# Kernel tuning notes

Hardware: AMD Instinct MI355X
Metric: run time of the kernel (lower is better)

Reference implementation:

```python
import jax, jax.numpy as jnp
import numpy as np

K = 20  # neighbors

def setup_inputs() -> dict:
    key = jax.random.key(0)
    k1, k2 = jax.random.split(key)
    B, C, N, O = 8, 64, 4096, 64
    x = jax.random.normal(k1, (B, C, N), dtype=jnp.float32)
    W = jax.random.normal(k2, (O, 2 * C), dtype=jnp.float32) * (1.0 / np.sqrt(2 * C))
    b = jnp.zeros((O,), dtype=jnp.float32)
    return {"x": x, "W": W, "b": b}

def _knn_idx(pts, k):
    # pts: [B, N, d]; returns [B, N, k] indices of k nearest neighbors (incl. self)
    sq = jnp.sum(pts * pts, axis=-1)                      # [B, N]
    inner = jnp.einsum('bnd,bmd->bnm', pts, pts)          # [B, N, N]
    neg_d2 = 2.0 * inner - sq[:, :, None] - sq[:, None, :]
    _, idx = jax.lax.top_k(neg_d2, k)                     # largest -dist = nearest
    return idx

def reference(x, W, b):
    # x: [B, C, N], W: [O, 2C], b: [O]
    pts = jnp.transpose(x, (0, 2, 1))                     # [B, N, C]
    idx = _knn_idx(jax.lax.stop_gradient(pts), K)         # [B, N, K]
    nbr = jax.vmap(lambda p, i: p[i])(pts, idx)           # [B, N, K, C]
    ctr = pts[:, :, None, :]                              # [B, N, 1, C]
    # local+global edge features: [diff, center] along channel dim -> [B, N, K, 2C]
    edge = jnp.concatenate([nbr - ctr, jnp.broadcast_to(ctr, nbr.shape)], axis=-1)
    # 1x1 conv == channel GEMM
    out = jnp.einsum('bnkc,oc->bonk', edge, W) + b[None, :, None, None]
    return jnp.max(out, axis=-1)                          # [B, O, N]
```

## Files before the change

### kernel.cpp

```cpp
#include <hip/hip_runtime.h>
#include <float.h>

typedef unsigned long long u64;
typedef unsigned int u32;
typedef unsigned short u16;

#define NPTS 4096
#define CDIM 64
#define BATCH 8
#define KSEL 20

#define F_XTL (BATCH * NPTS * 32)
#define F_CAND (2 * BATCH * NPTS * 32)
#define F_XTF (4 * BATCH * NPTS * 32)
#define F_SQ (6 * BATCH * NPTS * 32)
#define F_WT2 (F_SQ + BATCH * NPTS)
#define F_SQB (F_WT2 + 64 * 64)

typedef __attribute__((ext_vector_type(8))) short short8v;
typedef __attribute__((ext_vector_type(16))) float float16v;

#define MFMA32(a, b, c) __builtin_amdgcn_mfma_f32_32x32x16_bf16(a, b, c, 0, 0, 0)

__device__ __forceinline__ u32 ordf(float f) {
    u32 u = __float_as_uint(f);
    return (u >> 31) ? ~u : (u | 0x80000000u);
}
__device__ __forceinline__ u32 umaxu(u32 a, u32 b) { return a > b ? a : b; }
__device__ __forceinline__ u32 uminu(u32 a, u32 b) { return a < b ? a : b; }

__device__ __forceinline__ void load_lds_16(const void* g, void* l) {
    __builtin_amdgcn_global_load_lds(
        (const __attribute__((address_space(1))) unsigned int*)g,
        (__attribute__((address_space(3))) unsigned int*)l, 16, 0, 0);
}

#define CE(i, j) { u32 a_ = c[i], b_ = c[j]; c[i] = umaxu(a_, b_); c[j] = uminu(a_, b_); }

__device__ __forceinline__ void sort16_desc(u32 (&c)[16]) {
    CE(0,1) CE(2,3) CE(4,5) CE(6,7) CE(8,9) CE(10,11) CE(12,13) CE(14,15)
    CE(0,2) CE(1,3) CE(4,6) CE(5,7) CE(8,10) CE(9,11) CE(12,14) CE(13,15)
    CE(1,2) CE(5,6) CE(9,10) CE(13,14)
    CE(0,4) CE(1,5) CE(2,6) CE(3,7) CE(8,12) CE(9,13) CE(10,14) CE(11,15)
    CE(2,4) CE(3,5) CE(10,12) CE(11,13)
    CE(1,2) CE(3,4) CE(5,6) CE(9,10) CE(11,12) CE(13,14)
    CE(0,8) CE(1,9) CE(2,10) CE(3,11) CE(4,12) CE(5,13) CE(6,14) CE(7,15)
    CE(4,8) CE(5,9) CE(6,10) CE(7,11)
    CE(2,4) CE(3,5) CE(6,8) CE(7,9) CE(10,12) CE(11,13)
    CE(1,2) CE(3,4) CE(5,6) CE(7,8) CE(9,10) CE(11,12) CE(13,14)
}
#undef CE

__device__ __forceinline__ void merge_into16(u32 (&L)[16], const u32 (&c)[16]) {
#pragma unroll
    for (int i = 0; i < 16; i++) L[i] = umaxu(L[i], c[15 - i]);
#pragma unroll
    for (int j = 8; j >= 1; j >>= 1)
#pragma unroll
        for (int i = 0; i < 16; i++)
            if ((i & j) == 0) {
                int p = i | j;
                u32 a = L[i], b = L[p];
                L[i] = umaxu(a, b);
                L[p] = uminu(a, b);
            }
}

__global__ __launch_bounds__(256) void p1_prep(const float* __restrict__ x,
                                               const float* __restrict__ W,
                                               float* __restrict__ xtf,
                                               u16* __restrict__ xth,
                                               u16* __restrict__ xtl,
                                               float* __restrict__ sq,
                                               float* __restrict__ sqb,
                                               float* __restrict__ wt2g) {
    __shared__ float Xp[64][65];
    int tid = threadIdx.x;
    if (blockIdx.x >= 512) {
        int f = (blockIdx.x - 512) * 256 + tid;
        if (f < 64 * 64) {
            int c = f >> 6, o = f & 63;
            wt2g[f] = W[o * 128 + 64 + c] - W[o * 128 + c];
        }
        return;
    }
    int b = blockIdx.x >> 6;
    int n0 = (blockIdx.x & 63) * 64;
    const float* xb = x + (size_t)b * (CDIM * NPTS);
    int j = tid & 63, cq = tid >> 6;
#pragma unroll
    for (int i = 0; i < 16; i++) {
        int c = cq * 16 + i;
        Xp[c][j] = xb[(size_t)c * NPTS + n0 + j];
    }
    __syncthreads();
    if (tid < 64) {
        float s = 0.f;
        for (int c = 0; c < 64; c++) { float v = Xp[c][tid]; s = fmaf(v, v, s); }
        sq[(size_t)b * NPTS + n0 + tid] = s;
        sqb[(size_t)b * NPTS + n0 + tid] = 1024.f - s;
    }
    int n = tid >> 2, c0 = (tid & 3) * 16;
    float vv[16];
#pragma unroll
    for (int i = 0; i < 16; i++) vv[i] = Xp[c0 + i][n];
    size_t rowb = ((size_t)b * NPTS + n0 + n) * 64 + c0;
#pragma unroll
    for (int q = 0; q < 4; q++) {
        float4 f;
        f.x = vv[4 * q]; f.y = vv[4 * q + 1]; f.z = vv[4 * q + 2]; f.w = vv[4 * q + 3];
        *(float4*)(xtf + rowb + 4 * q) = f;
    }
    u16 hb[16], lb[16];
#pragma unroll
    for (int i = 0; i < 16; i++) {
        float v = vv[i] * 1.41421356237f;
        u32 bv = __float_as_uint(v);
        u32 h = (bv + 0x7FFFu + ((bv >> 16) & 1u)) >> 16;
        float hf = __uint_as_float(h << 16);
        float lf = v - hf;
        u32 bl = __float_as_uint(lf);
        u32 lo = (bl + 0x7FFFu + ((bl >> 16) & 1u)) >> 16;
        hb[i] = (u16)h; lb[i] = (u16)lo;
    }
    uint4 H0, H1, L0, L1;
    H0.x = hb[0] | ((u32)hb[1] << 16);  H0.y = hb[2] | ((u32)hb[3] << 16);
    H0.z = hb[4] | ((u32)hb[5] << 16);  H0.w = hb[6] | ((u32)hb[7] << 16);
    H1.x = hb[8] | ((u32)hb[9] << 16);  H1.y = hb[10] | ((u32)hb[11] << 16);
    H1.z = hb[12] | ((u32)hb[13] << 16); H1.w = hb[14] | ((u32)hb[15] << 16);
    L0.x = lb[0] | ((u32)lb[1] << 16);  L0.y = lb[2] | ((u32)lb[3] << 16);
    L0.z = lb[4] | ((u32)lb[5] << 16);  L0.w = lb[6] | ((u32)lb[7] << 16);
    L1.x = lb[8] | ((u32)lb[9] << 16);  L1.y = lb[10] | ((u32)lb[11] << 16);
    L1.z = lb[12] | ((u32)lb[13] << 16); L1.w = lb[14] | ((u32)lb[15] << 16);
    *(uint4*)(xth + rowb) = H0;
    *(uint4*)(xth + rowb + 8) = H1;
    *(uint4*)(xtl + rowb) = L0;
    *(uint4*)(xtl + rowb + 8) = L1;
}

__device__ __forceinline__ void stage_tile(const u16* __restrict__ srcb,
                                           char* lds, int w, int lane) {
#pragma unroll
    for (int i = 0; i < 2; i++) {
        int G = w * 128 + i * 64 + lane;
        int rr = G >> 3, gp = G & 7;
        const u16* src = srcb + rr * 64 + ((gp ^ (rr & 7)) << 3);
        char* dst = lds + (w * 128 + i * 64) * 16;
        load_lds_16(src, dst);
    }
}

__device__ __forceinline__ void sel_half(const float16v& A, int colbase2,
                                         u32 (&L)[16]) {
    u32 c[16];
#pragma unroll
    for (int q = 0; q < 4; q++) {
        u32 cg = (u32)(colbase2 + 8 * q);
        c[4 * q + 0] = (__float_as_uint(A[4 * q + 0]) & 0xFFFFF000u) | (cg + 0);
        c[4 * q + 1] = (__float_as_uint(A[4 * q + 1]) & 0xFFFFF000u) | (cg + 1);
        c[4 * q + 2] = (__float_as_uint(A[4 * q + 2]) & 0xFFFFF000u) | (cg + 2);
        c[4 * q + 3] = (__float_as_uint(A[4 * q + 3]) & 0xFFFFF000u) | (cg + 3);
    }
    sort16_desc(c);
    merge_into16(L, c);
}

__global__ __launch_bounds__(256, 4) void k2_gram(const u16* __restrict__ xth,
                                                  const u16* __restrict__ xtl,
                                                  const float* __restrict__ sqb,
                                                  u32* __restrict__ cand) {
    __shared__ char pool[8192];
    int tid = threadIdx.x;
    int lane = tid & 63, w = tid >> 6;
    int l31 = lane & 31, lh = lane >> 5;
    int b = blockIdx.x & 7;
    int rt = (blockIdx.x >> 3) & 31;
    int ch = blockIdx.x >> 8;
    int r0 = rt * 128;
    int cb = ch * 1024;
    size_t bbase = (size_t)b * NPTS;

    short8v Ah[4], Al[4];
    {
        const u16* pa = xth + (bbase + r0 + 32 * w + l31) * 64 + 8 * lh;
        const u16* pl = xtl + (bbase + r0 + 32 * w + l31) * 64 + 8 * lh;
#pragma unroll
        for (int s = 0; s < 4; s++) {
            Ah[s] = *(const short8v*)(pa + 16 * s);
            Al[s] = *(const short8v*)(pl + 16 * s);
        }
    }

    u32 L[16];
#pragma unroll
    for (int i = 0; i < 16; i++) L[i] = 0u;

    stage_tile(xth + (bbase + cb) * 64, pool, w, lane);
    __syncthreads();

    for (int t = 0; t < 16; t++) {
        int n1 = cb + t * 64;
        const float* sqbp = sqb + bbase + n1 + 4 * lh;

        float16v a0, a1;
#pragma unroll
        for (int q = 0; q < 4; q++) {
            ((float4*)&a0)[q] = *(const float4*)(sqbp + 8 * q);
            ((float4*)&a1)[q] = *(const float4*)(sqbp + 32 + 8 * q);
        }

#pragma unroll
        for (int s = 0; s < 4; s++) {
            int gx = 2 * s + lh;
            int sw = (gx ^ (l31 & 7)) << 4;
            short8v bh0 = *(const short8v*)(pool + l31 * 128 + sw);
            a0 = MFMA32(bh0, Ah[s], a0);
            a0 = MFMA32(bh0, Al[s], a0);
        }
        sel_half(a0, n1 + 4 * lh, L);

#pragma unroll
        for (int s = 0; s < 4; s++) {
            int gx = 2 * s + lh;
            int sw = (gx ^ (l31 & 7)) << 4;
            short8v bh1 = *(const short8v*)(pool + (32 + l31) * 128 + sw);
            a1 = MFMA32(bh1, Ah[s], a1);
            a1 = MFMA32(bh1, Al[s], a1);
        }
        __syncthreads();
        if (t < 15)
            stage_tile(xth + (bbase + n1 + 64) * 64, pool, w, lane);
        sel_half(a1, n1 + 32 + 4 * lh, L);
        __syncthreads();
    }

    u32 M[16];
#pragma unroll
    for (int i = 0; i < 16; i++) {
        u32 pv = __shfl_xor(L[15 - i], 32);
        M[i] = umaxu(L[i], pv);
    }
#pragma unroll
    for (int j = 8; j >= 1; j >>= 1)
#pragma unroll
        for (int i = 0; i < 16; i++)
            if ((i & j) == 0) {
                int p = i | j;
                u32 a = M[i], b2 = M[p];
                M[i] = umaxu(a, b2);
                M[p] = uminu(a, b2);
            }
    if (lane < 32) {
        u32* cr = cand + (bbase + r0 + 32 * w + l31) * 64 + ch * 16;
#pragma unroll
        for (int q = 0; q < 4; q++) {
            uint4 v;
            v.x = M[4 * q]; v.y = M[4 * q + 1]; v.z = M[4 * q + 2]; v.w = M[4 * q + 3];
            *(uint4*)(cr + 4 * q) = v;
        }
    }
}

__global__ __launch_bounds__(256) void k1_prep(const float* __restrict__ x,
                                               const float* __restrict__ W,
                                               float* __restrict__ y1) {
    __shared__ float Xt[64][128];
    __shared__ float Wt[64][64];
    int tid = threadIdx.x;
    int gr0 = blockIdx.x * 128;
    int b = gr0 >> 12;
    int n0 = gr0 & 4095;
    const float* xb = x + (size_t)b * (CDIM * NPTS) + n0;

    for (int k = 0; k < 32; k++) {
        int f = tid + 256 * k;
        int c = f >> 7, j = f & 127;
        Xt[c][j] = xb[(size_t)c * NPTS + j];
    }
    for (int k = 0; k < 16; k++) {
        int f = tid + 256 * k;
        int c = f >> 6, o = f & 63;
        Wt[c][o] = W[o * 128 + c];
    }
    __syncthreads();

    int tr = tid & 15, tc = tid >> 4;
    float acc[8][4];
#pragma unroll
    for (int i = 0; i < 8; i++)
#pragma unroll
        for (int j = 0; j < 4; j++) acc[i][j] = 0.f;

#pragma unroll 4
    for (int c = 0; c < 64; c++) {
        float a[8], bb[4];
        *(float4*)&a[0] = *(const float4*)&Xt[c][8 * tr];
        *(float4*)&a[4] = *(const float4*)&Xt[c][8 * tr + 4];
        *(float4*)&bb[0] = *(const float4*)&Wt[c][4 * tc];
#pragma unroll
        for (int i = 0; i < 8; i++)
#pragma unroll
            for (int j = 0; j < 4; j++) acc[i][j] = fmaf(a[i], bb[j], acc[i][j]);
    }

#pragma unroll
    for (int i = 0; i < 8; i++) {
        int r = gr0 + 8 * tr + i;
        float4 s0;
        s0.x = acc[i][0]; s0.y = acc[i][1]; s0.z = acc[i][2]; s0.w = acc[i][3];
        *(float4*)(y1 + (size_t)r * 64 + 4 * tc) = s0;
    }
}

__global__ __launch_bounds__(256) void k2b3(const float* __restrict__ xtf,
                                            const float* __restrict__ sq,
                                            const u32* __restrict__ cand,
                                            const float* __restrict__ y1,
                                            const float* __restrict__ wt2g,
                                            const float* __restrict__ bias,
                                            float* __restrict__ out) {
    __shared__ float wt2[64][64];
    __shared__ float xr[4][64];
    __shared__ float dd[4][32];
    __shared__ u32 cols[4][32];
    __shared__ int ids[4][KSEL];
    __shared__ float outT[64][5];
    int tid = threadIdx.x;
    int lane = tid & 63, w = tid >> 6;
    int bid = blockIdx.x;
    int b = bid & 7;
    int n0 = (bid >> 3) * 4;
    int n = n0 + w;
    size_t row = (size_t)b * NPTS + n;
    size_t bbase = (size_t)b * NPTS;

#pragma unroll
    for (int k = 0; k < 4; k++) {
        int f = tid + 256 * k;
        ((float4*)wt2)[f] = ((const float4*)wt2g)[f];
    }
    if (lane < 16)
        *(float4*)&xr[w][lane * 4] = *(const float4*)(xtf + row * 64 + lane * 4);
    u32 key = cand[row * 64 + lane];
    __syncthreads();

#pragma unroll
    for (u32 k = 2; k <= 64; k <<= 1) {
#pragma unroll
        for (u32 j2 = k >> 1; j2 >= 1; j2 >>= 1) {
            bool up = ((lane & k) == 0);
            bool lower = ((lane & j2) == 0);
            u32 p = __shfl_xor(key, j2);
            u32 mx = (key > p) ? key : p, mn = (key > p) ? p : key;
            key = (lower == up) ? mx : mn;
        }
    }
    if (lane < 32) cols[w][lane] = key & 0xFFFu;

    int s = lane & 3, g = lane >> 2;
    float4 xq[4];
#pragma unroll
    for (int q = 0; q < 4; q++) xq[q] = *(const float4*)&xr[w][16 * q + 4 * s];

#pragma unroll
    for (int p = 0; p < 2; p++) {
        int m = cols[w][p * 16 + g];
        const float* pm = xtf + (bbase + m) * 64;
        float d = 0.f;
#pragma unroll
        for (int q = 0; q < 4; q++) {
            float4 v = *(const float4*)(pm + 16 * q + 4 * s);
            d = fmaf(v.x, xq[q].x, d); d = fmaf(v.y, xq[q].y, d);
            d = fmaf(v.z, xq[q].z, d); d = fmaf(v.w, xq[q].w, d);
        }
        d += __shfl_xor(d, 1);
        d += __shfl_xor(d, 2);
        if (s == 0) dd[w][p * 16 + g] = d;
    }

    u64 kE = 0;
    if (lane < 32) {
        int m = (int)cols[w][lane];
        float sE = fmaf(2.f, dd[w][lane], -sq[bbase + m]);
        kE = ((u64)ordf(sE) << 32) | (u32)(~(u32)m);
    }
#pragma unroll
    for (u32 k = 2; k <= 32; k <<= 1) {
#pragma unroll
        for (u32 j2 = k >> 1; j2 >= 1; j2 >>= 1) {
            bool up = ((lane & k) == 0);
            bool lower = ((lane & j2) == 0);
            u64 p = __shfl_xor(kE, j2);
            u64 mx = (kE > p) ? kE : p, mn = (kE > p) ? p : kE;
            kE = (lower == up) ? mx : mn;
        }
    }
    if (lane < KSEL) ids[w][lane] = (int)(~(u32)kE);

    const float* y1b = y1 + bbase * 64;
    float acc = -FLT_MAX;
#pragma unroll
    for (int k = 0; k < KSEL; k++) {
        int m = ids[w][k];
        acc = fmaxf(acc, y1b[(size_t)m * 64 + lane]);
    }
    float acc2 = 0.f;
#pragma unroll 8
    for (int c = 0; c < 64; c++)
        acc2 = fmaf(xr[w][c], wt2[c][lane], acc2);
    outT[lane][w] = acc + acc2 + bias[lane];
    __syncthreads();

    if (tid < 64) {
        float4 v;
        v.x = outT[tid][0]; v.y = outT[tid][1];
        v.z = outT[tid][2]; v.w = outT[tid][3];
        *(float4*)(out + ((size_t)(b * 64 + tid)) * NPTS + n0) = v;
    }
}

extern "C" void kernel_launch(void* const* d_in, const int* in_sizes, int n_in,
                              void* d_out, int out_size, void* d_ws, size_t ws_size,
                              hipStream_t stream) {
    const float* x    = (const float*)d_in[0];
    const float* W    = (const float*)d_in[1];
    const float* bias = (const float*)d_in[2];
    float* out = (float*)d_out;
    float* ws = (float*)d_ws;

    u16* xth    = (u16*)ws;
    u16* xtl    = (u16*)(ws + F_XTL);
    u32* candb  = (u32*)(ws + F_CAND);
    float* xtf  = ws + F_XTF;
    float* sq   = ws + F_SQ;
    float* wt2g = ws + F_WT2;
    float* sqb  = ws + F_SQB;
    float* y1   = ws;

    hipLaunchKernelGGL(p1_prep, dim3(528),  dim3(256), 0, stream,
                       x, W, xtf, xth, xtl, sq, sqb, wt2g);
    hipLaunchKernelGGL(k2_gram, dim3(1024), dim3(256), 0, stream, xth, xtl, sqb, candb);
    hipLaunchKernelGGL(k1_prep, dim3(256),  dim3(256), 0, stream, x, W, y1);
    hipLaunchKernelGGL(k2b3,    dim3(8192), dim3(256), 0, stream,
                       xtf, sq, candb, y1, wt2g, bias, out);
}
```

Measured before the change: 142.3 us.

## Double-buffer gram tile staging and batch 16 points per refine block

In the gram kernel, the B tile moves to a double-buffered shared pool, so the next tile is loaded before the MFMAs on the current one and one barrier per iteration goes away. The final kernel now handles 16 points per block (4 per wave, in a loop), which cuts the grid to a quarter and amortises the 16 KB weight staging in shared memory. The 64-key bitonic sort of candidates becomes a reverse, a 32-wide bitonic merge and a max step, relying on the two 32-lane halves already being sorted. The risks are doubled LDS use in the gram kernel, which could lower occupancy, and a serial per-wave loop in the final kernel.

```diff
diff --git a/kernel.cpp b/kernel.cpp
--- a/kernel.cpp
+++ b/kernel.cpp
@@ -169,7 +169,7 @@
                                                   const u16* __restrict__ xtl,
                                                   const float* __restrict__ sqb,
                                                   u32* __restrict__ cand) {
-    __shared__ char pool[8192];
+    __shared__ char pool[2][8192];
     int tid = threadIdx.x;
     int lane = tid & 63, w = tid >> 6;
     int l31 = lane & 31, lh = lane >> 5;
@@ -195,13 +195,16 @@
 #pragma unroll
     for (int i = 0; i < 16; i++) L[i] = 0u;
 
-    stage_tile(xth + (bbase + cb) * 64, pool, w, lane);
+    stage_tile(xth + (bbase + cb) * 64, pool[0], w, lane);
     __syncthreads();
 
     for (int t = 0; t < 16; t++) {
         int n1 = cb + t * 64;
+        const char* pb = pool[t & 1];
+        if (t < 15)
+            stage_tile(xth + (bbase + n1 + 64) * 64, pool[(t + 1) & 1], w, lane);
+
         const float* sqbp = sqb + bbase + n1 + 4 * lh;
-
         float16v a0, a1;
 #pragma unroll
         for (int q = 0; q < 4; q++) {
@@ -213,7 +216,7 @@
         for (int s = 0; s < 4; s++) {
             int gx = 2 * s + lh;
             int sw = (gx ^ (l31 & 7)) << 4;
-            short8v bh0 = *(const short8v*)(pool + l31 * 128 + sw);
+            short8v bh0 = *(const short8v*)(pb + l31 * 128 + sw);
             a0 = MFMA32(bh0, Ah[s], a0);
             a0 = MFMA32(bh0, Al[s], a0);
         }
@@ -223,14 +226,12 @@
         for (int s = 0; s < 4; s++) {
             int gx = 2 * s + lh;
             int sw = (gx ^ (l31 & 7)) << 4;
-            short8v bh1 = *(const short8v*)(pool + (32 + l31) * 128 + sw);
+            short8v bh1 = *(const short8v*)(pb + (32 + l31) * 128 + sw);
             a1 = MFMA32(bh1, Ah[s], a1);
             a1 = MFMA32(bh1, Al[s], a1);
         }
-        __syncthreads();
-        if (t < 15)
-            stage_tile(xth + (bbase + n1 + 64) * 64, pool, w, lane);
         sel_half(a1, n1 + 32 + 4 * lh, L);
+
         __syncthreads();
     }
 
@@ -324,14 +325,12 @@
     __shared__ float dd[4][32];
     __shared__ u32 cols[4][32];
     __shared__ int ids[4][KSEL];
-    __shared__ float outT[64][5];
+    __shared__ float outT[64][17];
     int tid = threadIdx.x;
     int lane = tid & 63, w = tid >> 6;
     int bid = blockIdx.x;
     int b = bid & 7;
-    int n0 = (bid >> 3) * 4;
-    int n = n0 + w;
-    size_t row = (size_t)b * NPTS + n;
+    int nblk = (bid >> 3) * 16;
     size_t bbase = (size_t)b * NPTS;
 
 #pragma unroll
@@ -339,83 +338,95 @@
         int f = tid + 256 * k;
         ((float4*)wt2)[f] = ((const float4*)wt2g)[f];
     }
-    if (lane < 16)
-        *(float4*)&xr[w][lane * 4] = *(const float4*)(xtf + row * 64 + lane * 4);
-    u32 key = cand[row * 64 + lane];
     __syncthreads();
 
-#pragma unroll
-    for (u32 k = 2; k <= 64; k <<= 1) {
-#pragma unroll
-        for (u32 j2 = k >> 1; j2 >= 1; j2 >>= 1) {
-            bool up = ((lane & k) == 0);
-            bool lower = ((lane & j2) == 0);
+    int s = lane & 3, g = lane >> 2;
+    float bl = bias[lane];
+
+#pragma unroll 1
+    for (int i = 0; i < 4; i++) {
+        int n = nblk + w * 4 + i;
+        size_t row = bbase + n;
+
+        if (lane < 16)
+            *(float4*)&xr[w][lane * 4] = *(const float4*)(xtf + row * 64 + lane * 4);
+        u32 key = cand[row * 64 + lane];
+
+        int local = lane & 31;
+        {
+            int srcl = (local < 16) ? local : (47 - local);
+            key = __shfl(key, (lane & 32) | srcl);
+        }
+#pragma unroll
+        for (u32 j2 = 16; j2 >= 1; j2 >>= 1) {
             u32 p = __shfl_xor(key, j2);
-            u32 mx = (key > p) ? key : p, mn = (key > p) ? p : key;
-            key = (lower == up) ? mx : mn;
-        }
-    }
-    if (lane < 32) cols[w][lane] = key & 0xFFFu;
-
-    int s = lane & 3, g = lane >> 2;
-    float4 xq[4];
-#pragma unroll
-    for (int q = 0; q < 4; q++) xq[q] = *(const float4*)&xr[w][16 * q + 4 * s];
-
-#pragma unroll
-    for (int p = 0; p < 2; p++) {
-        int m = cols[w][p * 16 + g];
-        const float* pm = xtf + (bbase + m) * 64;
-        float d = 0.f;
-#pragma unroll
-        for (int q = 0; q < 4; q++) {
-            float4 v = *(const float4*)(pm + 16 * q + 4 * s);
-            d = fmaf(v.x, xq[q].x, d); d = fmaf(v.y, xq[q].y, d);
-            d = fmaf(v.z, xq[q].z, d); d = fmaf(v.w, xq[q].w, d);
-        }
-        d += __shfl_xor(d, 1);
-        d += __shfl_xor(d, 2);
-        if (s == 0) dd[w][p * 16 + g] = d;
-    }
-
-    u64 kE = 0;
-    if (lane < 32) {
-        int m = (int)cols[w][lane];
-        float sE = fmaf(2.f, dd[w][lane], -sq[bbase + m]);
-        kE = ((u64)ordf(sE) << 32) | (u32)(~(u32)m);
-    }
-#pragma unroll
-    for (u32 k = 2; k <= 32; k <<= 1) {
-#pragma unroll
-        for (u32 j2 = k >> 1; j2 >= 1; j2 >>= 1) {
-            bool up = ((lane & k) == 0);
-            bool lower = ((lane & j2) == 0);
-            u64 p = __shfl_xor(kE, j2);
-            u64 mx = (kE > p) ? kE : p, mn = (kE > p) ? p : kE;
-            kE = (lower == up) ? mx : mn;
-        }
-    }
-    if (lane < KSEL) ids[w][lane] = (int)(~(u32)kE);
-
-    const float* y1b = y1 + bbase * 64;
-    float acc = -FLT_MAX;
-#pragma unroll
-    for (int k = 0; k < KSEL; k++) {
-        int m = ids[w][k];
-        acc = fmaxf(acc, y1b[(size_t)m * 64 + lane]);
-    }
-    float acc2 = 0.f;
+            key = ((local & j2) == 0) ? umaxu(key, p) : uminu(key, p);
+        }
+        {
+            u32 p = __shfl(key, 63 - lane);
+            if (lane < 32) cols[w][lane] = umaxu(key, p) & 0xFFFu;
+        }
+
+        float4 xq[4];
+#pragma unroll
+        for (int q = 0; q < 4; q++) xq[q] = *(const float4*)&xr[w][16 * q + 4 * s];
+
+#pragma unroll
+        for (int p = 0; p < 2; p++) {
+            int m = cols[w][p * 16 + g];
+            const float* pm = xtf + (bbase + m) * 64;
+            float d = 0.f;
+#pragma unroll
+            for (int q = 0; q < 4; q++) {
+                float4 v = *(const float4*)(pm + 16 * q + 4 * s);
+                d = fmaf(v.x, xq[q].x, d); d = fmaf(v.y, xq[q].y, d);
+                d = fmaf(v.z, xq[q].z, d); d = fmaf(v.w, xq[q].w, d);
+            }
+            d += __shfl_xor(d, 1);
+            d += __shfl_xor(d, 2);
+            if (s == 0) dd[w][p * 16 + g] = d;
+        }
+
+        u64 kE = 0;
+        if (lane < 32) {
+            int m = (int)cols[w][lane];
+            float sE = fmaf(2.f, dd[w][lane], -sq[bbase + m]);
+            kE = ((u64)ordf(sE) << 32) | (u32)(~(u32)m);
+        }
+#pragma unroll
+        for (u32 k = 2; k <= 32; k <<= 1) {
+#pragma unroll
+            for (u32 j2 = k >> 1; j2 >= 1; j2 >>= 1) {
+                bool up = ((lane & k) == 0);
+                bool lower = ((lane & j2) == 0);
+                u64 p = __shfl_xor(kE, j2);
+                u64 mx = (kE > p) ? kE : p, mn = (kE > p) ? p : kE;
+                kE = (lower == up) ? mx : mn;
+            }
+        }
+        if (lane < KSEL) ids[w][lane] = (int)(~(u32)kE);
+
+        const float* y1b = y1 + bbase * 64;
+        float acc = -FLT_MAX;
+#pragma unroll
+        for (int k = 0; k < KSEL; k++) {
+            int m = ids[w][k];
+            acc = fmaxf(acc, y1b[(size_t)m * 64 + lane]);
+        }
+        float acc2 = 0.f;
 #pragma unroll 8
-    for (int c = 0; c < 64; c++)
-        acc2 = fmaf(xr[w][c], wt2[c][lane], acc2);
-    outT[lane][w] = acc + acc2 + bias[lane];
+        for (int c = 0; c < 64; c++)
+            acc2 = fmaf(xr[w][c], wt2[c][lane], acc2);
+        outT[lane][w * 4 + i] = acc + acc2 + bl;
+    }
     __syncthreads();
 
-    if (tid < 64) {
+    {
+        int o = tid & 63, q = tid >> 6;
         float4 v;
-        v.x = outT[tid][0]; v.y = outT[tid][1];
-        v.z = outT[tid][2]; v.w = outT[tid][3];
-        *(float4*)(out + ((size_t)(b * 64 + tid)) * NPTS + n0) = v;
+        v.x = outT[o][q * 4 + 0]; v.y = outT[o][q * 4 + 1];
+        v.z = outT[o][q * 4 + 2]; v.w = outT[o][q * 4 + 3];
+        *(float4*)(out + ((size_t)(b * 64 + o)) * NPTS + nblk + q * 4) = v;
     }
 }
 
@@ -441,6 +452,6 @@
                        x, W, xtf, xth, xtl, sq, sqb, wt2g);
     hipLaunchKernelGGL(k2_gram, dim3(1024), dim3(256), 0, stream, xth, xtl, sqb, candb);
     hipLaunchKernelGGL(k1_prep, dim3(256),  dim3(256), 0, stream, x, W, y1);
-    hipLaunchKernelGGL(k2b3,    dim3(8192), dim3(256), 0, stream,
+    hipLaunchKernelGGL(k2b3,    dim3(2048), dim3(256), 0, stream,
                        xtf, sq, candb, y1, wt2g, bias, out);
 }
```

Measured after the change: 141.7 us. Within noise of the previous version (-0.4%).
